# Kernel optimization log

Hardware: AMD Instinct MI355X
Metric: run time of the kernel (lower is better)

## Reference

```python
import jax, jax.numpy as jnp
import numpy as np


def setup_inputs() -> dict:
    key = jax.random.key(0)
    ks = jax.random.split(key, 6)
    B, S, DK = 4, 2048, 1024
    scale = 1.0 / np.sqrt(DK)  # keep weight magnitudes sane like torch init
    return {
        "q": jax.random.normal(ks[0], (B, S, DK), jnp.float32),
        "k": jax.random.normal(ks[1], (B, S, DK), jnp.float32),
        "v": jax.random.normal(ks[2], (B, S, DK), jnp.float32),
        "wq": jax.random.normal(ks[3], (DK, DK), jnp.float32) * scale,
        "wk": jax.random.normal(ks[4], (DK, DK), jnp.float32) * scale,
        "wv": jax.random.normal(ks[5], (DK, DK), jnp.float32) * scale,
    }


def reference(q, k, v, wq, wk, wv):
    dk = q.shape[-1]
    # nn.Linear: y = x @ W^T  (weights stored [out, in])
    qp = jnp.einsum("bsd,ed->bse", q, wq)
    kp = jnp.einsum("bsd,ed->bse", k, wk)
    vp = jnp.einsum("bsd,ed->bse", v, wv)
    norm = 1.0 / jnp.sqrt(jnp.asarray(dk, qp.dtype))
    s = jnp.einsum("bqd,bkd->bqk", qp, kp) * norm  # [B, S, S]
    # module computes exp(s)/sum(exp(s)) manually; mathematically softmax
    e = jnp.exp(s)
    attention = e / jnp.sum(e, axis=-1, keepdims=True)
    # dropout is identity in eval mode (deterministic reference)
    return jnp.einsum("bqk,bkd->bqd", attention, vp)
```

## Files before the change

kernel.cpp:

```cpp
#include <hip/hip_runtime.h>

typedef _Float16 f16;
typedef _Float16 f16x4 __attribute__((ext_vector_type(4)));
typedef _Float16 f16x8 __attribute__((ext_vector_type(8)));
typedef float    fx4   __attribute__((ext_vector_type(4)));

#define MODE_PROJ   0
#define MODE_SCORES 1
#define MODE_PV     2

constexpr int Bsz = 4;
constexpr int S   = 2048;
constexpr int DK  = 1024;
constexpr int BM = 128, BN = 256, BK = 64;
constexpr long SD   = (long)S * DK;
constexpr long SS   = (long)S * S;
constexpr long BIGN = (long)Bsz * S * DK;

__device__ __forceinline__ void glds16(const f16* g, f16* l) {
    __builtin_amdgcn_global_load_lds(
        (const __attribute__((address_space(1))) void*)g,
        (__attribute__((address_space(3))) void*)l, 16, 0, 0);
}

__global__ __launch_bounds__(256)
void convert_kernel(const float* q, const float* k, const float* v,
                    const float* wq, const float* wk, const float* wv)
{
    int bx = blockIdx.x;
    const float* src;
    int blk;
    if (bx < 12288) {
        int t = bx >> 12; blk = bx & 4095;
        src = (t == 0) ? q : (t == 1) ? k : v;
    } else {
        int u = bx - 12288;
        int t = u >> 9; blk = u & 511;
        src = (t == 0) ? wq : (t == 1) ? wk : wv;
    }
    size_t off = (size_t)blk * 2048 + (size_t)threadIdx.x * 8;
    float4 f0 = *(const float4*)(src + off);
    float4 f1 = *(const float4*)(src + off + 4);
    __syncthreads();
    f16x8 h = {(f16)f0.x, (f16)f0.y, (f16)f0.z, (f16)f0.w,
               (f16)f1.x, (f16)f1.y, (f16)f1.z, (f16)f1.w};
    *(f16x8*)((char*)src + (size_t)blk * 8192 + (size_t)threadIdx.x * 16) = h;
}

__device__ __forceinline__ size_t pp(int r, int c) {
    return ((size_t)(r >> 1) << 12) + ((r & 1) << 10) + c;
}

template<int MODE>
__global__ __launch_bounds__(512, 2)
void gemm_kernel(const f16* A0, const f16* A1, const f16* A2,
                 const f16* B0, const f16* B1, const f16* B2,
                 void* O0, void* O1, float* rowsum,
                 int lda, int ldb, int K, int ldo)
{
    __shared__ __attribute__((aligned(16))) f16 lA[2][BM * BK];
    __shared__ __attribute__((aligned(16))) f16 lB[2][BN * BK];

    const int tid = threadIdx.x;
    const int id  = blockIdx.x;
    const int z   = blockIdx.y;
    int row0, col0;
    if constexpr (MODE == MODE_PROJ) { row0 = (id & 63) * BM; col0 = (id >> 6) * BN; }
    else                             { row0 = (id & 15) * BM; col0 = (id >> 4) * BN; }

    const int lane = tid & 63;
    const int quad = lane >> 4;
    const int cn   = lane & 15;
    const int w    = tid >> 6;
    const int wm   = w >> 2;
    const int wn   = w & 3;

    const f16 *Ap, *Bp;
    if constexpr (MODE == MODE_PROJ) {
        Ap = (z == 0) ? A0 : (z == 1) ? A1 : A2;
        Bp = (z == 0) ? B0 : (z == 1) ? B1 : B2;
    } else if constexpr (MODE == MODE_SCORES) {
        Ap = A0 + (long)z * SD;  Bp = B0 + (long)z * SD;
        rowsum += (long)z * S;
    } else {
        Ap = A0 + (long)z * SS;  Bp = B0 + (long)z * SD;
        rowsum += (long)z * S;
    }

    fx4 acc[4][4];
    #pragma unroll
    for (int mt = 0; mt < 4; ++mt)
        #pragma unroll
        for (int nt = 0; nt < 4; ++nt)
            acc[mt][nt] = (fx4){0.f, 0.f, 0.f, 0.f};

    const int lr8 = lane >> 3;
    const int swc = (lane & 7) ^ lr8;
    const int lcS = swc << 3;

    f16x8 af[4];
    f16x8 bf[8];

#define STAGE(BUF, K0) do {                                                          \
    _Pragma("unroll")                                                                \
    for (int i_ = 0; i_ < 2; ++i_) {                                                 \
        int rb_ = w * 16 + i_ * 8;                                                   \
        if constexpr (MODE == MODE_PROJ)                                             \
            glds16(Ap + pp(row0 + rb_ + lr8, (K0) + lcS), &lA[BUF][rb_ * BK]);       \
        else                                                                         \
            glds16(Ap + (size_t)(row0 + rb_ + lr8) * lda + (K0) + lcS,               \
                   &lA[BUF][rb_ * BK]);                                              \
    }                                                                                \
    _Pragma("unroll")                                                                \
    for (int i_ = 0; i_ < 4; ++i_) {                                                 \
        int rb_ = w * 32 + i_ * 8;                                                   \
        if constexpr (MODE == MODE_PROJ)                                             \
            glds16(Bp + pp(col0 + rb_ + lr8, (K0) + lcS), &lB[BUF][rb_ * BK]);       \
        else                                                                         \
            glds16(Bp + (size_t)(col0 + rb_ + lr8) * ldb + (K0) + lcS,               \
                   &lB[BUF][rb_ * BK]);                                              \
    }                                                                                \
} while (0)

#define LDA_FRAGS(BUF, MH) do {                                                      \
    _Pragma("unroll")                                                                \
    for (int m_ = 0; m_ < 2; ++m_)                                                   \
        _Pragma("unroll")                                                            \
        for (int kk_ = 0; kk_ < 2; ++kk_) {                                          \
            int r_  = wm * 64 + ((MH) * 2 + m_) * 16 + cn;                           \
            int ch_ = ((kk_ << 2) | quad) ^ (r_ & 7);                                \
            af[m_ * 2 + kk_] = *(const f16x8*)&lA[BUF][r_ * BK + ch_ * 8];           \
        }                                                                            \
} while (0)

#define LDB_FRAGS(BUF, NH) do {                                                      \
    _Pragma("unroll")                                                                \
    for (int n_ = 0; n_ < 2; ++n_)                                                   \
        _Pragma("unroll")                                                            \
        for (int kk_ = 0; kk_ < 2; ++kk_) {                                          \
            int nt_ = (NH) * 2 + n_;                                                 \
            int r_  = wn * 64 + nt_ * 16 + cn;                                       \
            int ch_ = ((kk_ << 2) | quad) ^ (r_ & 7);                                \
            bf[nt_ * 2 + kk_] = *(const f16x8*)&lB[BUF][r_ * BK + ch_ * 8];          \
        }                                                                            \
} while (0)

#define QUAD_MFMA(MH, NH) do {                                                       \
    __builtin_amdgcn_s_setprio(1);                                                   \
    _Pragma("unroll")                                                                \
    for (int m_ = 0; m_ < 2; ++m_)                                                   \
        _Pragma("unroll")                                                            \
        for (int n_ = 0; n_ < 2; ++n_) {                                             \
            _Pragma("unroll")                                                        \
            for (int kk_ = 0; kk_ < 2; ++kk_)                                        \
                acc[(MH) * 2 + m_][(NH) * 2 + n_] =                                  \
                    __builtin_amdgcn_mfma_f32_16x16x32_f16(                          \
                        af[m_ * 2 + kk_], bf[((NH) * 2 + n_) * 2 + kk_],             \
                        acc[(MH) * 2 + m_][(NH) * 2 + n_], 0, 0, 0);                 \
        }                                                                            \
    __builtin_amdgcn_s_setprio(0);                                                   \
} while (0)

    const int ntile = K / BK;
    STAGE(0, 0);
    __syncthreads();
    int bufc = 0;
    for (int t = 0; t < ntile; ++t) {
        const int k0 = t * BK;
        LDA_FRAGS(bufc, 0);
        LDB_FRAGS(bufc, 0);
        if (t + 1 < ntile) STAGE(bufc ^ 1, k0 + BK);
        __builtin_amdgcn_s_barrier();
        QUAD_MFMA(0, 0);
        __builtin_amdgcn_s_barrier();
        LDB_FRAGS(bufc, 1);
        __builtin_amdgcn_s_barrier();
        QUAD_MFMA(0, 1);
        __builtin_amdgcn_s_barrier();
        LDA_FRAGS(bufc, 1);
        __builtin_amdgcn_s_barrier();
        QUAD_MFMA(1, 1);
        __builtin_amdgcn_s_barrier();
        QUAD_MFMA(1, 0);
        __syncthreads();
        bufc ^= 1;
    }

#undef STAGE
#undef LDA_FRAGS
#undef LDB_FRAGS
#undef QUAD_MFMA

    if constexpr (MODE == MODE_PROJ) {
        if (z < 2) {
            f16* O = (f16*)O0 + (long)z * BIGN;
            #pragma unroll
            for (int mt = 0; mt < 4; ++mt) {
                int r0 = row0 + wm * 64 + mt * 16 + quad * 4;
                #pragma unroll
                for (int nt = 0; nt < 4; ++nt) {
                    int c = col0 + wn * 64 + nt * 16 + cn;
                    #pragma unroll
                    for (int reg = 0; reg < 4; ++reg)
                        O[(size_t)(r0 + reg) * DK + c] = (f16)acc[mt][nt][reg];
                }
            }
        } else {
            #pragma unroll
            for (int mt = 0; mt < 4; ++mt) {
                int r0 = row0 + wm * 64 + mt * 16 + quad * 4;
                int b  = r0 >> 11;
                int s  = r0 & 2047;
                f16* O = (f16*)O1 + (long)b * SD;
                #pragma unroll
                for (int nt = 0; nt < 4; ++nt) {
                    int c = col0 + wn * 64 + nt * 16 + cn;
                    f16x4 h = {(f16)acc[mt][nt][0], (f16)acc[mt][nt][1],
                               (f16)acc[mt][nt][2], (f16)acc[mt][nt][3]};
                    *(f16x4*)&O[(size_t)c * S + s] = h;
                }
            }
        }
    } else if constexpr (MODE == MODE_SCORES) {
        f16* O = (f16*)O0 + (long)z * SS;
        const float sl2e = 0.03125f * 1.44269504f;
        float rs[4][4];
        #pragma unroll
        for (int mt = 0; mt < 4; ++mt)
            #pragma unroll
            for (int reg = 0; reg < 4; ++reg) rs[mt][reg] = 0.f;
        #pragma unroll
        for (int mt = 0; mt < 4; ++mt) {
            int r0 = row0 + wm * 64 + mt * 16 + quad * 4;
            #pragma unroll
            for (int nt = 0; nt < 4; ++nt) {
                int c = col0 + wn * 64 + nt * 16 + cn;
                #pragma unroll
                for (int reg = 0; reg < 4; ++reg) {
                    float vv = exp2f(acc[mt][nt][reg] * sl2e);
                    rs[mt][reg] += vv;
                    O[(size_t)(r0 + reg) * ldo + c] = (f16)vv;
                }
            }
        }
        #pragma unroll
        for (int mt = 0; mt < 4; ++mt) {
            int r0 = row0 + wm * 64 + mt * 16 + quad * 4;
            #pragma unroll
            for (int reg = 0; reg < 4; ++reg) {
                float vv = rs[mt][reg];
                vv += __shfl_xor(vv, 1);
                vv += __shfl_xor(vv, 2);
                vv += __shfl_xor(vv, 4);
                vv += __shfl_xor(vv, 8);
                if (cn == 0) atomicAdd(&rowsum[r0 + reg], vv);
            }
        }
    } else {
        float* O = (float*)O0 + (long)z * SD;
        #pragma unroll
        for (int mt = 0; mt < 4; ++mt) {
            int r0 = row0 + wm * 64 + mt * 16 + quad * 4;
            fx4 rsv = *(const fx4*)&rowsum[r0];
            fx4 inv = {1.f / rsv[0], 1.f / rsv[1], 1.f / rsv[2], 1.f / rsv[3]};
            #pragma unroll
            for (int nt = 0; nt < 4; ++nt) {
                int c = col0 + wn * 64 + nt * 16 + cn;
                #pragma unroll
                for (int reg = 0; reg < 4; ++reg)
                    O[(size_t)(r0 + reg) * ldo + c] = acc[mt][nt][reg] * inv[reg];
            }
        }
    }
}

extern "C" void kernel_launch(void* const* d_in, const int* in_sizes, int n_in,
                              void* d_out, int out_size, void* d_ws, size_t ws_size,
                              hipStream_t stream) {
    const float* q  = (const float*)d_in[0];
    const float* k  = (const float*)d_in[1];
    const float* v  = (const float*)d_in[2];
    const float* wq = (const float*)d_in[3];
    const float* wk = (const float*)d_in[4];
    const float* wv = (const float*)d_in[5];
    float* out = (float*)d_out;

    char* ws = (char*)d_ws;
    f16*   qp     = (f16*)(ws);
    f16*   kp     = (f16*)(ws + ((size_t)16 << 20));
    f16*   vpT    = (f16*)(ws + ((size_t)32 << 20));
    f16*   E      = (f16*)(ws + ((size_t)48 << 20));
    float* rowsum = (float*)(ws + ((size_t)80 << 20));

    hipMemsetAsync(rowsum, 0, (size_t)Bsz * S * sizeof(float), stream);

    convert_kernel<<<13824, 256, 0, stream>>>(q, k, v, wq, wk, wv);

    const f16* qh  = (const f16*)q;
    const f16* kh  = (const f16*)k;
    const f16* vh  = (const f16*)v;
    const f16* wqh = (const f16*)wq;
    const f16* wkh = (const f16*)wk;
    const f16* wvh = (const f16*)wv;

    dim3 blk(512);
    gemm_kernel<MODE_PROJ><<<dim3(256, 3), blk, 0, stream>>>(
        qh, kh, vh, wqh, wkh, wvh, qp, vpT, nullptr, DK, DK, DK, DK);
    gemm_kernel<MODE_SCORES><<<dim3(128, 4), blk, 0, stream>>>(
        qp, nullptr, nullptr, kp, nullptr, nullptr, E, nullptr, rowsum,
        DK, DK, DK, S);
    gemm_kernel<MODE_PV><<<dim3(64, 4), blk, 0, stream>>>(
        E, nullptr, nullptr, vpT, nullptr, nullptr, out, nullptr, rowsum,
        S, S, S, DK);
}
```

Measured before the change: 309.0 us.

## Triple-buffer LDS tiles and spread global prefetch across MFMA phases

Moves the GEMM main loop from double to triple buffering in LDS, prefetching the tile two iterations ahead. The B-tile loads are split into halves and interleaved between the MFMA quadrants, and explicit vmcnt waits replace the full __syncthreads so loads stay in flight across iterations. The goal is to hide global memory latency better, at the cost of 50% more LDS (144KB per block with 512 threads), which may cut occupancy from two blocks to one per CU.

```diff
diff --git a/kernel.cpp b/kernel.cpp
--- a/kernel.cpp
+++ b/kernel.cpp
@@ -58,8 +58,8 @@
                  void* O0, void* O1, float* rowsum,
                  int lda, int ldb, int K, int ldo)
 {
-    __shared__ __attribute__((aligned(16))) f16 lA[2][BM * BK];
-    __shared__ __attribute__((aligned(16))) f16 lB[2][BN * BK];
+    __shared__ __attribute__((aligned(16))) f16 lA[3][BM * BK];
+    __shared__ __attribute__((aligned(16))) f16 lB[3][BN * BK];
 
     const int tid = threadIdx.x;
     const int id  = blockIdx.x;
@@ -101,7 +101,7 @@
     f16x8 af[4];
     f16x8 bf[8];
 
-#define STAGE(BUF, K0) do {                                                          \
+#define STAGE_A(BUF, K0) do {                                                        \
     _Pragma("unroll")                                                                \
     for (int i_ = 0; i_ < 2; ++i_) {                                                 \
         int rb_ = w * 16 + i_ * 8;                                                   \
@@ -111,9 +111,12 @@
             glds16(Ap + (size_t)(row0 + rb_ + lr8) * lda + (K0) + lcS,               \
                    &lA[BUF][rb_ * BK]);                                              \
     }                                                                                \
-    _Pragma("unroll")                                                                \
-    for (int i_ = 0; i_ < 4; ++i_) {                                                 \
-        int rb_ = w * 32 + i_ * 8;                                                   \
+} while (0)
+
+#define STAGE_B(BUF, K0, H) do {                                                     \
+    _Pragma("unroll")                                                                \
+    for (int i_ = 0; i_ < 2; ++i_) {                                                 \
+        int rb_ = w * 32 + ((H) * 2 + i_) * 8;                                       \
         if constexpr (MODE == MODE_PROJ)                                             \
             glds16(Bp + pp(col0 + rb_ + lr8, (K0) + lcS), &lB[BUF][rb_ * BK]);       \
         else                                                                         \
@@ -162,31 +165,43 @@
 } while (0)
 
     const int ntile = K / BK;
-    STAGE(0, 0);
-    __syncthreads();
-    int bufc = 0;
+    STAGE_A(0, 0);  STAGE_B(0, 0, 0);  STAGE_B(0, 0, 1);
+    STAGE_A(1, BK); STAGE_B(1, BK, 0); STAGE_B(1, BK, 1);
+    asm volatile("s_waitcnt vmcnt(6)" ::: "memory");
+    __builtin_amdgcn_s_barrier();
+
+    int cb = 0;
     for (int t = 0; t < ntile; ++t) {
-        const int k0 = t * BK;
-        LDA_FRAGS(bufc, 0);
-        LDB_FRAGS(bufc, 0);
-        if (t + 1 < ntile) STAGE(bufc ^ 1, k0 + BK);
+        int sb = cb + 2; if (sb >= 3) sb -= 3;
+        const bool pf = (t + 2 < ntile);
+        const int kpf = (t + 2) * BK;
+        LDA_FRAGS(cb, 0);
+        LDB_FRAGS(cb, 0);
+        if (pf) STAGE_A(sb, kpf);
         __builtin_amdgcn_s_barrier();
         QUAD_MFMA(0, 0);
         __builtin_amdgcn_s_barrier();
-        LDB_FRAGS(bufc, 1);
+        LDB_FRAGS(cb, 1);
+        if (pf) STAGE_B(sb, kpf, 0);
         __builtin_amdgcn_s_barrier();
         QUAD_MFMA(0, 1);
         __builtin_amdgcn_s_barrier();
-        LDA_FRAGS(bufc, 1);
+        LDA_FRAGS(cb, 1);
+        if (pf) STAGE_B(sb, kpf, 1);
         __builtin_amdgcn_s_barrier();
         QUAD_MFMA(1, 1);
         __builtin_amdgcn_s_barrier();
         QUAD_MFMA(1, 0);
-        __syncthreads();
-        bufc ^= 1;
+        if (t + 1 < ntile) {
+            if (pf) asm volatile("s_waitcnt vmcnt(6)" ::: "memory");
+            else    asm volatile("s_waitcnt vmcnt(0)" ::: "memory");
+            __builtin_amdgcn_s_barrier();
+        }
+        cb = cb + 1; if (cb >= 3) cb -= 3;
     }
 
-#undef STAGE
+#undef STAGE_A
+#undef STAGE_B
 #undef LDA_FRAGS
 #undef LDB_FRAGS
 #undef QUAD_MFMA
```

Result: slower. 329.1 us (+6.5%).
